# Kernel tuning notes

Hardware: AMD Instinct MI355X
Metric: run time of the kernel (lower is better)

Reference implementation:

```python
import jax, jax.numpy as jnp
import numpy as np

N_NODES = 50000
N_EDGES = 600000
D_IN = 128
D_HID = 128
D_OUT = 128
LN_EPS = 1e-5


def _layer_norm(h, g, b):
    mu = jnp.mean(h, axis=-1, keepdims=True)
    var = jnp.var(h, axis=-1, keepdims=True)
    return (h - mu) * jax.lax.rsqrt(var + LN_EPS) * g + b


def _gin_conv(x, src, dst, w1, b1, w2, b2):
    # sum-aggregate neighbor messages at destination nodes, eps = 0
    agg = jax.ops.segment_sum(x[src], dst, num_segments=x.shape[0])
    h = x + agg
    h = jax.nn.relu(h @ w1 + b1)
    return h @ w2 + b2


def setup_inputs() -> dict:
    key = jax.random.key(0)
    ks = jax.random.split(key, 20)
    x = jax.random.normal(ks[0], (N_NODES, D_IN), dtype=jnp.float32)
    edge_index = jax.random.randint(ks[1], (2, N_EDGES), 0, N_NODES, dtype=jnp.int64)
    dims = [(D_IN, D_HID), (D_HID, D_HID), (D_HID, D_HID), (D_HID, D_OUT)]
    inp = {"x": x, "edge_index": edge_index}
    for i, (din, dout) in enumerate(dims):
        s1 = 1.0 / np.sqrt(din)
        s2 = 1.0 / np.sqrt(D_HID)
        inp[f"w1_{i}"] = jax.random.uniform(ks[2 + 4 * i], (din, D_HID), jnp.float32, -s1, s1)
        inp[f"b1_{i}"] = jax.random.uniform(ks[3 + 4 * i], (D_HID,), jnp.float32, -s1, s1)
        inp[f"w2_{i}"] = jax.random.uniform(ks[4 + 4 * i], (D_HID, dout), jnp.float32, -s2, s2)
        inp[f"b2_{i}"] = jax.random.uniform(ks[5 + 4 * i], (dout,), jnp.float32, -s2, s2)
    for i in range(3):  # LayerNorm only on first 3 blocks
        inp[f"g_{i}"] = jnp.ones((D_HID,), jnp.float32)
        inp[f"beta_{i}"] = jnp.zeros((D_HID,), jnp.float32)
    return inp


def reference(x, edge_index,
              w1_0, b1_0, w2_0, b2_0,
              w1_1, b1_1, w2_1, b2_1,
              w1_2, b1_2, w2_2, b2_2,
              w1_3, b1_3, w2_3, b2_3,
              g_0, beta_0, g_1, beta_1, g_2, beta_2):
    src, dst = edge_index[0], edge_index[1]
    mlps = [(w1_0, b1_0, w2_0, b2_0), (w1_1, b1_1, w2_1, b2_1),
            (w1_2, b1_2, w2_2, b2_2), (w1_3, b1_3, w2_3, b2_3)]
    lns = [(g_0, beta_0), (g_1, beta_1), (g_2, beta_2)]
    h = x
    for i in range(3):
        h = _gin_conv(h, src, dst, *mlps[i])
        h = _layer_norm(h, *lns[i])
        h = jax.nn.relu(h)  # dropout rate 0.0 -> identity
    h = _gin_conv(h, src, dst, *mlps[3])  # final block: no norm/act
    return h
```

## Files before the change

### kernel.cpp

```cpp
#include <hip/hip_runtime.h>
#include <hip/hip_bf16.h>

#define NN 50000
#define NE 600000
#define DD 128
#define LDSW 136
#define SC 256
#define NCH ((NN + SC - 1) / SC)

typedef __bf16 bf16;
typedef __attribute__((ext_vector_type(8))) __bf16 bf16x8;
typedef __attribute__((ext_vector_type(4))) float f32x4;
typedef __attribute__((ext_vector_type(4))) unsigned int u32x4;
typedef __attribute__((ext_vector_type(4))) unsigned short u16x4;
typedef unsigned short u16;

__device__ __forceinline__ float bf_lo(unsigned int u) {
    return __builtin_bit_cast(float, u << 16);
}
__device__ __forceinline__ float bf_hi(unsigned int u) {
    return __builtin_bit_cast(float, u & 0xffff0000u);
}
__device__ __forceinline__ unsigned int bf_pack(float x, float y) {
    u16 a = __builtin_bit_cast(u16, (bf16)x);
    u16 b = __builtin_bit_cast(u16, (bf16)y);
    return (unsigned int)a | ((unsigned int)b << 16);
}

struct Ptr8 { const float* p[8]; };

__device__ __forceinline__ int edge_dst(const int* ei, int e, int f) {
    return f ? ei[2 * NE + 2 * e] : ei[NE + e];
}
__device__ __forceinline__ int edge_src(const int* ei, int e, int f) {
    return f ? ei[2 * e] : ei[e];
}

#define J0 50000
#define J1 (J0 + NN * DD / 4)
#define J2 (J1 + 8 * DD * DD)

__global__ __launch_bounds__(256) void k_init(const float* __restrict__ x,
                                              u16* __restrict__ xb,
                                              Ptr8 ws, u16* __restrict__ wt,
                                              int* __restrict__ deg,
                                              const int* __restrict__ ei,
                                              int* __restrict__ flag) {
    int tid = threadIdx.x;
    if (blockIdx.x == 0) {
        if (tid == 0) flag[0] = 1;
        __syncthreads();
        if (ei[2 * tid + 1] != 0) flag[0] = 0;
    }
    int id = blockIdx.x * 256 + tid;
    if (id < J0) {
        deg[id] = 0;
    } else if (id < J1) {
        int i = id - J0;
        f32x4 v = *(const f32x4*)(x + (size_t)i * 4);
        u16x4 o;
        o.x = __builtin_bit_cast(u16, (bf16)v.x);
        o.y = __builtin_bit_cast(u16, (bf16)v.y);
        o.z = __builtin_bit_cast(u16, (bf16)v.z);
        o.w = __builtin_bit_cast(u16, (bf16)v.w);
        *(u16x4*)(xb + (size_t)i * 4) = o;
    } else if (id < J2) {
        int i = id - J1;
        int m = i >> 14;
        int rem = i & 16383;
        int k = rem >> 7;
        int n = rem & 127;
        bf16 b = (bf16)ws.p[m][k * DD + n];
        wt[(size_t)m * DD * DD + n * DD + k] = __builtin_bit_cast(u16, b);
    }
}

__global__ void k_degree(const int* __restrict__ ei, const int* __restrict__ flag,
                         int* __restrict__ deg) {
    int i = blockIdx.x * blockDim.x + threadIdx.x;
    if (i < NE) {
        int f = flag[0];
        atomicAdd(&deg[edge_dst(ei, i, f)], 1);
    }
}

__global__ __launch_bounds__(256) void k_scan1(const int* __restrict__ deg,
                                               int* __restrict__ partial) {
    int b = blockIdx.x, tid = threadIdx.x;
    int i = b * SC + tid;
    int v = (i < NN) ? deg[i] : 0;
#pragma unroll
    for (int off = 1; off < 64; off <<= 1) v += __shfl_xor(v, off);
    __shared__ int sm[4];
    if ((tid & 63) == 0) sm[tid >> 6] = v;
    __syncthreads();
    if (tid == 0) partial[b] = sm[0] + sm[1] + sm[2] + sm[3];
}

__global__ __launch_bounds__(256) void k_scan2(const int* __restrict__ partial,
                                               int* __restrict__ chunk_off) {
    int tid = threadIdx.x;
    int lane = tid & 63, w = tid >> 6;
    int v = (tid < NCH) ? partial[tid] : 0;
    int orig = v;
#pragma unroll
    for (int off = 1; off < 64; off <<= 1) {
        int t = __shfl_up(v, off);
        if (lane >= off) v += t;
    }
    __shared__ int sm[4];
    if (lane == 63) sm[w] = v;
    __syncthreads();
    int add = 0;
    for (int k = 0; k < w; k++) add += sm[k];
    v += add;
    if (tid < NCH) chunk_off[tid] = v - orig;
}

__global__ __launch_bounds__(256) void k_scan3(const int* __restrict__ deg,
                                               const int* __restrict__ chunk_off,
                                               int* __restrict__ row_start,
                                               int* __restrict__ cursor) {
    int b = blockIdx.x, tid = threadIdx.x;
    int i = b * SC + tid;
    int lane = tid & 63, w = tid >> 6;
    int v = (i < NN) ? deg[i] : 0;
    int orig = v;
#pragma unroll
    for (int off = 1; off < 64; off <<= 1) {
        int t = __shfl_up(v, off);
        if (lane >= off) v += t;
    }
    __shared__ int sm[4];
    if (lane == 63) sm[w] = v;
    __syncthreads();
    int add = chunk_off[b];
    for (int k = 0; k < w; k++) add += sm[k];
    int ex = v - orig + add;
    if (i < NN) { row_start[i] = ex; cursor[i] = ex; }
    if (b == 0 && tid == 0) row_start[NN] = NE;
}

__global__ void k_fill(const int* __restrict__ ei, const int* __restrict__ flag,
                       int* __restrict__ cursor, int* __restrict__ adj) {
    int i = blockIdx.x * blockDim.x + threadIdx.x;
    if (i < NE) {
        int f = flag[0];
        int d = edge_dst(ei, i, f);
        int p = atomicAdd(&cursor[d], 1);
        adj[p] = edge_src(ei, i, f);
    }
}

__global__ __launch_bounds__(256) void k_agg(const u16* __restrict__ xb,
                                             const int* __restrict__ row_start,
                                             const int* __restrict__ adj,
                                             u16* __restrict__ out) {
    int gid = blockIdx.x * blockDim.x + threadIdx.x;
    int wave = gid >> 6, lane = gid & 63;
    int g = lane >> 4, l = lane & 15;
    int node = wave * 4 + g;
    if (node >= NN) return;
    const u32x4* base = (const u32x4*)xb;
    u32x4 sv = base[(size_t)node * 16 + l];
    float af[8];
#pragma unroll
    for (int j = 0; j < 4; j++) { af[2 * j] = bf_lo(sv[j]); af[2 * j + 1] = bf_hi(sv[j]); }
    int s = row_start[node], e = row_start[node + 1];
    int i = s;
    for (; i + 1 < e; i += 2) {
        u32x4 t0 = base[(size_t)adj[i] * 16 + l];
        u32x4 t1 = base[(size_t)adj[i + 1] * 16 + l];
#pragma unroll
        for (int j = 0; j < 4; j++) {
            af[2 * j]     += bf_lo(t0[j]) + bf_lo(t1[j]);
            af[2 * j + 1] += bf_hi(t0[j]) + bf_hi(t1[j]);
        }
    }
    if (i < e) {
        u32x4 t = base[(size_t)adj[i] * 16 + l];
#pragma unroll
        for (int j = 0; j < 4; j++) { af[2 * j] += bf_lo(t[j]); af[2 * j + 1] += bf_hi(t[j]); }
    }
    u32x4 o;
#pragma unroll
    for (int j = 0; j < 4; j++) o[j] = bf_pack(af[2 * j], af[2 * j + 1]);
    ((u32x4*)out)[(size_t)node * 16 + l] = o;
}

template <bool LN, bool B16OUT>
__global__ __launch_bounds__(256) void k_mlp(const u16* __restrict__ hin,
                                             const u16* __restrict__ w1t,
                                             const float* __restrict__ b1,
                                             const u16* __restrict__ w2t,
                                             const float* __restrict__ b2,
                                             const float* __restrict__ g,
                                             const float* __restrict__ bta,
                                             void* __restrict__ hout) {
    __shared__ u16 lds[128 * LDSW];
    const int tid = threadIdx.x;
    const int wv = tid >> 6, lane = tid & 63;
    const int l15 = lane & 15, l4 = lane >> 4;
    const int tile0 = blockIdx.x * 128;

#pragma unroll
    for (int it = 0; it < 8; ++it) {
        int slot = tid + it * 256;
        int row = slot >> 4, c16 = slot & 15;
        u32x4 v = {0u, 0u, 0u, 0u};
        int grow = tile0 + row;
        if (grow < NN) v = *(const u32x4*)(hin + (size_t)grow * DD + c16 * 8);
        *(u32x4*)&lds[row * LDSW + c16 * 8] = v;
    }
    __syncthreads();

    float b1c[8], b2c[8], gc[8], bc[8];
#pragma unroll
    for (int c = 0; c < 8; c++) {
        int col = c * 16 + l15;
        b1c[c] = b1[col];
        b2c[c] = b2[col];
        if (LN) { gc[c] = g[col]; bc[c] = bta[col]; }
    }

    f32x4 acc[2][8];
#pragma unroll
    for (int r = 0; r < 2; r++)
#pragma unroll
        for (int c = 0; c < 8; c++) acc[r][c] = (f32x4){0.f, 0.f, 0.f, 0.f};

    const int rowbase = wv * 32;

#pragma unroll
    for (int ks = 0; ks < 4; ++ks) {
        bf16x8 a0 = __builtin_bit_cast(bf16x8,
            *(const u32x4*)&lds[(rowbase + l15) * LDSW + ks * 32 + l4 * 8]);
        bf16x8 a1 = __builtin_bit_cast(bf16x8,
            *(const u32x4*)&lds[(rowbase + 16 + l15) * LDSW + ks * 32 + l4 * 8]);
#pragma unroll
        for (int c = 0; c < 8; c++) {
            bf16x8 b = __builtin_bit_cast(bf16x8,
                *(const u32x4*)(w1t + (size_t)(c * 16 + l15) * DD + ks * 32 + l4 * 8));
            acc[0][c] = __builtin_amdgcn_mfma_f32_16x16x32_bf16(a0, b, acc[0][c], 0, 0, 0);
            acc[1][c] = __builtin_amdgcn_mfma_f32_16x16x32_bf16(a1, b, acc[1][c], 0, 0, 0);
        }
    }

#pragma unroll
    for (int r = 0; r < 2; r++) {
#pragma unroll
        for (int c = 0; c < 8; c++) {
            int col = c * 16 + l15;
#pragma unroll
            for (int j = 0; j < 4; j++) {
                float v = acc[r][c][j] + b1c[c];
                v = v > 0.f ? v : 0.f;
                bf16 b = (bf16)v;
                int row = rowbase + r * 16 + l4 * 4 + j;
                lds[row * LDSW + col] = __builtin_bit_cast(u16, b);
            }
        }
    }
    __syncthreads();

#pragma unroll
    for (int r = 0; r < 2; r++)
#pragma unroll
        for (int c = 0; c < 8; c++) acc[r][c] = (f32x4){0.f, 0.f, 0.f, 0.f};

#pragma unroll
    for (int ks = 0; ks < 4; ++ks) {
        bf16x8 a0 = __builtin_bit_cast(bf16x8,
            *(const u32x4*)&lds[(rowbase + l15) * LDSW + ks * 32 + l4 * 8]);
        bf16x8 a1 = __builtin_bit_cast(bf16x8,
            *(const u32x4*)&lds[(rowbase + 16 + l15) * LDSW + ks * 32 + l4 * 8]);
#pragma unroll
        for (int c = 0; c < 8; c++) {
            bf16x8 b = __builtin_bit_cast(bf16x8,
                *(const u32x4*)(w2t + (size_t)(c * 16 + l15) * DD + ks * 32 + l4 * 8));
            acc[0][c] = __builtin_amdgcn_mfma_f32_16x16x32_bf16(a0, b, acc[0][c], 0, 0, 0);
            acc[1][c] = __builtin_amdgcn_mfma_f32_16x16x32_bf16(a1, b, acc[1][c], 0, 0, 0);
        }
    }

#pragma unroll
    for (int r = 0; r < 2; r++) {
        float vals[8][4];
#pragma unroll
        for (int c = 0; c < 8; c++)
#pragma unroll
            for (int j = 0; j < 4; j++) vals[c][j] = acc[r][c][j] + b2c[c];

        if (LN) {
            float s[4], q[4];
#pragma unroll
            for (int j = 0; j < 4; j++) {
                s[j] = 0.f; q[j] = 0.f;
#pragma unroll
                for (int c = 0; c < 8; c++) {
                    s[j] += vals[c][j];
                    q[j] += vals[c][j] * vals[c][j];
                }
            }
#pragma unroll
            for (int m = 1; m <= 8; m <<= 1) {
#pragma unroll
                for (int j = 0; j < 4; j++) {
                    s[j] += __shfl_xor(s[j], m);
                    q[j] += __shfl_xor(q[j], m);
                }
            }
#pragma unroll
            for (int j = 0; j < 4; j++) {
                float mu = s[j] * (1.f / 128.f);
                float var = q[j] * (1.f / 128.f) - mu * mu;
                float rs = rsqrtf(var + 1e-5f);
#pragma unroll
                for (int c = 0; c < 8; c++) {
                    float v = (vals[c][j] - mu) * rs * gc[c] + bc[c];
                    vals[c][j] = v > 0.f ? v : 0.f;
                }
            }
        }

#pragma unroll
        for (int c = 0; c < 8; c++) {
            int col = c * 16 + l15;
#pragma unroll
            for (int j = 0; j < 4; j++) {
                int row = tile0 + rowbase + r * 16 + l4 * 4 + j;
                if (row < NN) {
                    if (B16OUT) {
                        ((u16*)hout)[(size_t)row * DD + col] =
                            __builtin_bit_cast(u16, (bf16)vals[c][j]);
                    } else {
                        ((float*)hout)[(size_t)row * DD + col] = vals[c][j];
                    }
                }
            }
        }
    }
}

extern "C" void kernel_launch(void* const* d_in, const int* in_sizes, int n_in,
                              void* d_out, int out_size, void* d_ws, size_t ws_size,
                              hipStream_t stream) {
    const float* x = (const float*)d_in[0];
    const int* ei = (const int*)d_in[1];
    const float* w1[4]; const float* b1[4]; const float* w2[4]; const float* b2[4];
    for (int i = 0; i < 4; i++) {
        w1[i] = (const float*)d_in[2 + 4 * i];
        b1[i] = (const float*)d_in[3 + 4 * i];
        w2[i] = (const float*)d_in[4 + 4 * i];
        b2[i] = (const float*)d_in[5 + 4 * i];
    }
    const float* g[3]; const float* bt[3];
    for (int i = 0; i < 3; i++) {
        g[i] = (const float*)d_in[18 + 2 * i];
        bt[i] = (const float*)d_in[19 + 2 * i];
    }

    char* ws = (char*)d_ws;
    size_t off = 0;
    auto alloc = [&](size_t bytes) -> char* {
        char* p = ws + off;
        off = (off + bytes + 255) & ~(size_t)255;
        return p;
    };
    int* flag      = (int*)alloc(4);
    int* row_start = (int*)alloc((NN + 1) * 4);
    int* deg       = (int*)alloc(NN * 4);
    int* cursor    = (int*)alloc(NN * 4);
    int* adj       = (int*)alloc(NE * 4);
    int* partial   = (int*)alloc(NCH * 4);
    int* chunk_off = (int*)alloc(NCH * 4);
    u16* wt        = (u16*)alloc((size_t)8 * DD * DD * 2);
    u16* xb        = (u16*)alloc((size_t)NN * DD * 2);
    u16* hbf       = (u16*)alloc((size_t)NN * DD * 2);
    u16* hA        = (u16*)alloc((size_t)NN * DD * 2);
    u16* hB        = (u16*)alloc((size_t)NN * DD * 2);

    Ptr8 p8;
    for (int i = 0; i < 4; i++) {
        p8.p[2 * i] = w1[i];
        p8.p[2 * i + 1] = w2[i];
    }

    k_init<<<(J2 + 255) / 256, 256, 0, stream>>>(x, xb, p8, wt, deg, ei, flag);
    k_degree<<<(NE + 255) / 256, 256, 0, stream>>>(ei, flag, deg);
    k_scan1<<<NCH, 256, 0, stream>>>(deg, partial);
    k_scan2<<<1, 256, 0, stream>>>(partial, chunk_off);
    k_scan3<<<NCH, 256, 0, stream>>>(deg, chunk_off, row_start, cursor);
    k_fill<<<(NE + 255) / 256, 256, 0, stream>>>(ei, flag, cursor, adj);

    const u16* hin = xb;
    for (int i = 0; i < 4; i++) {
        k_agg<<<(NN / 4 * 64 + 255) / 256, 256, 0, stream>>>(hin, row_start, adj, hbf);
        const u16* w1ti = wt + (size_t)(2 * i) * DD * DD;
        const u16* w2ti = wt + (size_t)(2 * i + 1) * DD * DD;
        if (i < 3) {
            u16* outp = (i & 1) ? hB : hA;
            k_mlp<true, true><<<(NN + 127) / 128, 256, 0, stream>>>(
                hbf, w1ti, b1[i], w2ti, b2[i], g[i], bt[i], outp);
            hin = outp;
        } else {
            k_mlp<false, false><<<(NN + 127) / 128, 256, 0, stream>>>(
                hbf, w1ti, b1[i], w2ti, b2[i], nullptr, nullptr, d_out);
        }
    }
}
```

Measured before the change: 276.3 us.

## Fuse neighbor aggregation into MLP kernel, gathering directly into LDS

```diff
diff --git a/kernel.cpp b/kernel.cpp
--- a/kernel.cpp
+++ b/kernel.cpp
@@ -152,65 +152,61 @@
     }
 }
 
-__global__ __launch_bounds__(256) void k_agg(const u16* __restrict__ xb,
-                                             const int* __restrict__ row_start,
-                                             const int* __restrict__ adj,
-                                             u16* __restrict__ out) {
-    int gid = blockIdx.x * blockDim.x + threadIdx.x;
-    int wave = gid >> 6, lane = gid & 63;
-    int g = lane >> 4, l = lane & 15;
-    int node = wave * 4 + g;
-    if (node >= NN) return;
-    const u32x4* base = (const u32x4*)xb;
-    u32x4 sv = base[(size_t)node * 16 + l];
-    float af[8];
-#pragma unroll
-    for (int j = 0; j < 4; j++) { af[2 * j] = bf_lo(sv[j]); af[2 * j + 1] = bf_hi(sv[j]); }
-    int s = row_start[node], e = row_start[node + 1];
-    int i = s;
-    for (; i + 1 < e; i += 2) {
-        u32x4 t0 = base[(size_t)adj[i] * 16 + l];
-        u32x4 t1 = base[(size_t)adj[i + 1] * 16 + l];
-#pragma unroll
-        for (int j = 0; j < 4; j++) {
-            af[2 * j]     += bf_lo(t0[j]) + bf_lo(t1[j]);
-            af[2 * j + 1] += bf_hi(t0[j]) + bf_hi(t1[j]);
-        }
-    }
-    if (i < e) {
-        u32x4 t = base[(size_t)adj[i] * 16 + l];
-#pragma unroll
-        for (int j = 0; j < 4; j++) { af[2 * j] += bf_lo(t[j]); af[2 * j + 1] += bf_hi(t[j]); }
-    }
-    u32x4 o;
-#pragma unroll
-    for (int j = 0; j < 4; j++) o[j] = bf_pack(af[2 * j], af[2 * j + 1]);
-    ((u32x4*)out)[(size_t)node * 16 + l] = o;
-}
-
 template <bool LN, bool B16OUT>
-__global__ __launch_bounds__(256) void k_mlp(const u16* __restrict__ hin,
-                                             const u16* __restrict__ w1t,
-                                             const float* __restrict__ b1,
-                                             const u16* __restrict__ w2t,
-                                             const float* __restrict__ b2,
-                                             const float* __restrict__ g,
-                                             const float* __restrict__ bta,
-                                             void* __restrict__ hout) {
+__global__ __launch_bounds__(256) void k_fused(const u16* __restrict__ hin,
+                                               const int* __restrict__ row_start,
+                                               const int* __restrict__ adj,
+                                               const u16* __restrict__ w1t,
+                                               const float* __restrict__ b1,
+                                               const u16* __restrict__ w2t,
+                                               const float* __restrict__ b2,
+                                               const float* __restrict__ g,
+                                               const float* __restrict__ bta,
+                                               void* __restrict__ hout) {
     __shared__ u16 lds[128 * LDSW];
     const int tid = threadIdx.x;
     const int wv = tid >> 6, lane = tid & 63;
+    const int grp = lane >> 4, l = lane & 15;
     const int l15 = lane & 15, l4 = lane >> 4;
     const int tile0 = blockIdx.x * 128;
 
-#pragma unroll
-    for (int it = 0; it < 8; ++it) {
-        int slot = tid + it * 256;
-        int row = slot >> 4, c16 = slot & 15;
-        u32x4 v = {0u, 0u, 0u, 0u};
-        int grow = tile0 + row;
-        if (grow < NN) v = *(const u32x4*)(hin + (size_t)grow * DD + c16 * 8);
-        *(u32x4*)&lds[row * LDSW + c16 * 8] = v;
+    const u32x4* base = (const u32x4*)hin;
+#pragma unroll
+    for (int pass = 0; pass < 8; ++pass) {
+        int r = wv * 32 + pass * 4 + grp;
+        int node = tile0 + r;
+        float af[8], bf[8];
+#pragma unroll
+        for (int j = 0; j < 8; j++) { af[j] = 0.f; bf[j] = 0.f; }
+        if (node < NN) {
+            u32x4 sv = base[(size_t)node * 16 + l];
+#pragma unroll
+            for (int j = 0; j < 4; j++) { af[2 * j] = bf_lo(sv[j]); af[2 * j + 1] = bf_hi(sv[j]); }
+            int s = row_start[node], e = row_start[node + 1];
+            int i = s;
+            for (; i + 3 < e; i += 4) {
+                u32x4 t0 = base[(size_t)adj[i] * 16 + l];
+                u32x4 t1 = base[(size_t)adj[i + 1] * 16 + l];
+                u32x4 t2 = base[(size_t)adj[i + 2] * 16 + l];
+                u32x4 t3 = base[(size_t)adj[i + 3] * 16 + l];
+#pragma unroll
+                for (int j = 0; j < 4; j++) {
+                    af[2 * j]     += bf_lo(t0[j]) + bf_lo(t1[j]);
+                    af[2 * j + 1] += bf_hi(t0[j]) + bf_hi(t1[j]);
+                    bf[2 * j]     += bf_lo(t2[j]) + bf_lo(t3[j]);
+                    bf[2 * j + 1] += bf_hi(t2[j]) + bf_hi(t3[j]);
+                }
+            }
+            for (; i < e; i++) {
+                u32x4 t = base[(size_t)adj[i] * 16 + l];
+#pragma unroll
+                for (int j = 0; j < 4; j++) { af[2 * j] += bf_lo(t[j]); af[2 * j + 1] += bf_hi(t[j]); }
+            }
+        }
+        u32x4 o;
+#pragma unroll
+        for (int j = 0; j < 4; j++) o[j] = bf_pack(af[2 * j] + bf[2 * j], af[2 * j + 1] + bf[2 * j + 1]);
+        *(u32x4*)&lds[r * LDSW + l * 8] = o;
     }
     __syncthreads();
 
@@ -376,7 +372,6 @@
     int* chunk_off = (int*)alloc(NCH * 4);
     u16* wt        = (u16*)alloc((size_t)8 * DD * DD * 2);
     u16* xb        = (u16*)alloc((size_t)NN * DD * 2);
-    u16* hbf       = (u16*)alloc((size_t)NN * DD * 2);
     u16* hA        = (u16*)alloc((size_t)NN * DD * 2);
     u16* hB        = (u16*)alloc((size_t)NN * DD * 2);
 
@@ -393,19 +388,19 @@
     k_scan3<<<NCH, 256, 0, stream>>>(deg, chunk_off, row_start, cursor);
     k_fill<<<(NE + 255) / 256, 256, 0, stream>>>(ei, flag, cursor, adj);
 
+    const int grid = (NN + 127) / 128;
     const u16* hin = xb;
     for (int i = 0; i < 4; i++) {
-        k_agg<<<(NN / 4 * 64 + 255) / 256, 256, 0, stream>>>(hin, row_start, adj, hbf);
         const u16* w1ti = wt + (size_t)(2 * i) * DD * DD;
         const u16* w2ti = wt + (size_t)(2 * i + 1) * DD * DD;
         if (i < 3) {
             u16* outp = (i & 1) ? hB : hA;
-            k_mlp<true, true><<<(NN + 127) / 128, 256, 0, stream>>>(
-                hbf, w1ti, b1[i], w2ti, b2[i], g[i], bt[i], outp);
+            k_fused<true, true><<<grid, 256, 0, stream>>>(
+                hin, row_start, adj, w1ti, b1[i], w2ti, b2[i], g[i], bt[i], outp);
             hin = outp;
         } else {
-            k_mlp<false, false><<<(NN + 127) / 128, 256, 0, stream>>>(
-                hbf, w1ti, b1[i], w2ti, b2[i], nullptr, nullptr, d_out);
-        }
-    }
-}
+            k_fused<false, false><<<grid, 256, 0, stream>>>(
+                hin, row_start, adj, w1ti, b1[i], w2ti, b2[i], nullptr, nullptr, d_out);
+        }
+    }
+}
```

After: 322.7 us. 16.8% more time.

## Sort nodes by degree for aggregation and unroll gather loop by four

Applied to the files above, without the earlier changes.

```diff
diff --git a/kernel.cpp b/kernel.cpp
--- a/kernel.cpp
+++ b/kernel.cpp
@@ -7,6 +7,7 @@
 #define LDSW 136
 #define SC 256
 #define NCH ((NN + SC - 1) / SC)
+#define NBIN 64
 
 typedef __bf16 bf16;
 typedef __attribute__((ext_vector_type(8))) __bf16 bf16x8;
@@ -44,6 +45,7 @@
                                               u16* __restrict__ xb,
                                               Ptr8 ws, u16* __restrict__ wt,
                                               int* __restrict__ deg,
+                                              int* __restrict__ hist,
                                               const int* __restrict__ ei,
                                               int* __restrict__ flag) {
     int tid = threadIdx.x;
@@ -53,6 +55,7 @@
         if (ei[2 * tid + 1] != 0) flag[0] = 0;
     }
     int id = blockIdx.x * 256 + tid;
+    if (id < NBIN) hist[id] = 0;
     if (id < J0) {
         deg[id] = 0;
     } else if (id < J1) {
@@ -85,20 +88,32 @@
 }
 
 __global__ __launch_bounds__(256) void k_scan1(const int* __restrict__ deg,
-                                               int* __restrict__ partial) {
+                                               int* __restrict__ partial,
+                                               int* __restrict__ hist) {
     int b = blockIdx.x, tid = threadIdx.x;
     int i = b * SC + tid;
     int v = (i < NN) ? deg[i] : 0;
-#pragma unroll
-    for (int off = 1; off < 64; off <<= 1) v += __shfl_xor(v, off);
+    __shared__ int lh[NBIN];
+    if (tid < NBIN) lh[tid] = 0;
+    __syncthreads();
+    if (i < NN) {
+        int d = v > (NBIN - 1) ? (NBIN - 1) : v;
+        atomicAdd(&lh[d], 1);
+    }
+    int s = v;
+#pragma unroll
+    for (int off = 1; off < 64; off <<= 1) s += __shfl_xor(s, off);
     __shared__ int sm[4];
-    if ((tid & 63) == 0) sm[tid >> 6] = v;
+    if ((tid & 63) == 0) sm[tid >> 6] = s;
     __syncthreads();
     if (tid == 0) partial[b] = sm[0] + sm[1] + sm[2] + sm[3];
+    if (tid < NBIN && lh[tid] > 0) atomicAdd(&hist[tid], lh[tid]);
 }
 
 __global__ __launch_bounds__(256) void k_scan2(const int* __restrict__ partial,
-                                               int* __restrict__ chunk_off) {
+                                               int* __restrict__ chunk_off,
+                                               const int* __restrict__ hist,
+                                               int* __restrict__ dcur) {
     int tid = threadIdx.x;
     int lane = tid & 63, w = tid >> 6;
     int v = (tid < NCH) ? partial[tid] : 0;
@@ -115,12 +130,24 @@
     for (int k = 0; k < w; k++) add += sm[k];
     v += add;
     if (tid < NCH) chunk_off[tid] = v - orig;
+    if (tid < NBIN) {
+        int h = hist[tid];
+        int hv = h;
+#pragma unroll
+        for (int off = 1; off < 64; off <<= 1) {
+            int t = __shfl_up(hv, off);
+            if (lane >= off) hv += t;
+        }
+        dcur[tid] = hv - h;
+    }
 }
 
 __global__ __launch_bounds__(256) void k_scan3(const int* __restrict__ deg,
                                                const int* __restrict__ chunk_off,
                                                int* __restrict__ row_start,
-                                               int* __restrict__ cursor) {
+                                               int* __restrict__ cursor,
+                                               int* __restrict__ dcur,
+                                               int* __restrict__ perm) {
     int b = blockIdx.x, tid = threadIdx.x;
     int i = b * SC + tid;
     int lane = tid & 63, w = tid >> 6;
@@ -139,6 +166,20 @@
     int ex = v - orig + add;
     if (i < NN) { row_start[i] = ex; cursor[i] = ex; }
     if (b == 0 && tid == 0) row_start[NN] = NE;
+
+    __shared__ int lh[NBIN];
+    __shared__ int gb[NBIN];
+    if (tid < NBIN) lh[tid] = 0;
+    __syncthreads();
+    int d = 0, lpos = 0;
+    if (i < NN) {
+        d = orig > (NBIN - 1) ? (NBIN - 1) : orig;
+        lpos = atomicAdd(&lh[d], 1);
+    }
+    __syncthreads();
+    if (tid < NBIN && lh[tid] > 0) gb[tid] = atomicAdd(&dcur[tid], lh[tid]);
+    __syncthreads();
+    if (i < NN) perm[gb[d] + lpos] = i;
 }
 
 __global__ void k_fill(const int* __restrict__ ei, const int* __restrict__ flag,
@@ -155,36 +196,44 @@
 __global__ __launch_bounds__(256) void k_agg(const u16* __restrict__ xb,
                                              const int* __restrict__ row_start,
                                              const int* __restrict__ adj,
+                                             const int* __restrict__ perm,
                                              u16* __restrict__ out) {
     int gid = blockIdx.x * blockDim.x + threadIdx.x;
     int wave = gid >> 6, lane = gid & 63;
-    int g = lane >> 4, l = lane & 15;
-    int node = wave * 4 + g;
-    if (node >= NN) return;
+    int grp = lane >> 4, l = lane & 15;
+    int slot = wave * 4 + grp;
+    int node = perm[slot];
     const u32x4* base = (const u32x4*)xb;
     u32x4 sv = base[(size_t)node * 16 + l];
-    float af[8];
-#pragma unroll
-    for (int j = 0; j < 4; j++) { af[2 * j] = bf_lo(sv[j]); af[2 * j + 1] = bf_hi(sv[j]); }
+    float af[8], bf[8];
+#pragma unroll
+    for (int j = 0; j < 4; j++) {
+        af[2 * j] = bf_lo(sv[j]); af[2 * j + 1] = bf_hi(sv[j]);
+        bf[2 * j] = 0.f; bf[2 * j + 1] = 0.f;
+    }
     int s = row_start[node], e = row_start[node + 1];
     int i = s;
-    for (; i + 1 < e; i += 2) {
+    for (; i + 3 < e; i += 4) {
         u32x4 t0 = base[(size_t)adj[i] * 16 + l];
         u32x4 t1 = base[(size_t)adj[i + 1] * 16 + l];
+        u32x4 t2 = base[(size_t)adj[i + 2] * 16 + l];
+        u32x4 t3 = base[(size_t)adj[i + 3] * 16 + l];
 #pragma unroll
         for (int j = 0; j < 4; j++) {
             af[2 * j]     += bf_lo(t0[j]) + bf_lo(t1[j]);
             af[2 * j + 1] += bf_hi(t0[j]) + bf_hi(t1[j]);
-        }
-    }
-    if (i < e) {
+            bf[2 * j]     += bf_lo(t2[j]) + bf_lo(t3[j]);
+            bf[2 * j + 1] += bf_hi(t2[j]) + bf_hi(t3[j]);
+        }
+    }
+    for (; i < e; i++) {
         u32x4 t = base[(size_t)adj[i] * 16 + l];
 #pragma unroll
         for (int j = 0; j < 4; j++) { af[2 * j] += bf_lo(t[j]); af[2 * j + 1] += bf_hi(t[j]); }
     }
     u32x4 o;
 #pragma unroll
-    for (int j = 0; j < 4; j++) o[j] = bf_pack(af[2 * j], af[2 * j + 1]);
+    for (int j = 0; j < 4; j++) o[j] = bf_pack(af[2 * j] + bf[2 * j], af[2 * j + 1] + bf[2 * j + 1]);
     ((u32x4*)out)[(size_t)node * 16 + l] = o;
 }
 
@@ -374,6 +423,9 @@
     int* adj       = (int*)alloc(NE * 4);
     int* partial   = (int*)alloc(NCH * 4);
     int* chunk_off = (int*)alloc(NCH * 4);
+    int* hist      = (int*)alloc(NBIN * 4);
+    int* dcur      = (int*)alloc(NBIN * 4);
+    int* perm      = (int*)alloc(NN * 4);
     u16* wt        = (u16*)alloc((size_t)8 * DD * DD * 2);
     u16* xb        = (u16*)alloc((size_t)NN * DD * 2);
     u16* hbf       = (u16*)alloc((size_t)NN * DD * 2);
@@ -386,16 +438,16 @@
         p8.p[2 * i + 1] = w2[i];
     }
 
-    k_init<<<(J2 + 255) / 256, 256, 0, stream>>>(x, xb, p8, wt, deg, ei, flag);
+    k_init<<<(J2 + 255) / 256, 256, 0, stream>>>(x, xb, p8, wt, deg, hist, ei, flag);
     k_degree<<<(NE + 255) / 256, 256, 0, stream>>>(ei, flag, deg);
-    k_scan1<<<NCH, 256, 0, stream>>>(deg, partial);
-    k_scan2<<<1, 256, 0, stream>>>(partial, chunk_off);
-    k_scan3<<<NCH, 256, 0, stream>>>(deg, chunk_off, row_start, cursor);
+    k_scan1<<<NCH, 256, 0, stream>>>(deg, partial, hist);
+    k_scan2<<<1, 256, 0, stream>>>(partial, chunk_off, hist, dcur);
+    k_scan3<<<NCH, 256, 0, stream>>>(deg, chunk_off, row_start, cursor, dcur, perm);
     k_fill<<<(NE + 255) / 256, 256, 0, stream>>>(ei, flag, cursor, adj);
 
     const u16* hin = xb;
     for (int i = 0; i < 4; i++) {
-        k_agg<<<(NN / 4 * 64 + 255) / 256, 256, 0, stream>>>(hin, row_start, adj, hbf);
+        k_agg<<<(NN / 4 * 64) / 256, 256, 0, stream>>>(hin, row_start, adj, perm, hbf);
         const u16* w1ti = wt + (size_t)(2 * i) * DD * DD;
         const u16* w2ti = wt + (size_t)(2 * i + 1) * DD * DD;
         if (i < 3) {
```

Result: no change. 276.6 us (+0.1%).

## Build CSR via two-level bucket sort instead of global atomic degree counting

Applied to the files above, without the earlier changes.

```diff
diff --git a/kernel.cpp b/kernel.cpp
--- a/kernel.cpp
+++ b/kernel.cpp
@@ -5,8 +5,10 @@
 #define NE 600000
 #define DD 128
 #define LDSW 136
-#define SC 256
-#define NCH ((NN + SC - 1) / SC)
+#define NB 196
+#define BSH 8
+#define EPB 2048
+#define NBLK_AC ((NE + EPB - 1) / EPB)
 
 typedef __bf16 bf16;
 typedef __attribute__((ext_vector_type(8))) __bf16 bf16x8;
@@ -36,14 +38,13 @@
     return f ? ei[2 * e] : ei[e];
 }
 
-#define J0 50000
-#define J1 (J0 + NN * DD / 4)
+#define J1 (NN * DD / 4)
 #define J2 (J1 + 8 * DD * DD)
 
 __global__ __launch_bounds__(256) void k_init(const float* __restrict__ x,
                                               u16* __restrict__ xb,
                                               Ptr8 ws, u16* __restrict__ wt,
-                                              int* __restrict__ deg,
+                                              int* __restrict__ bcnt,
                                               const int* __restrict__ ei,
                                               int* __restrict__ flag) {
     int tid = threadIdx.x;
@@ -53,17 +54,15 @@
         if (ei[2 * tid + 1] != 0) flag[0] = 0;
     }
     int id = blockIdx.x * 256 + tid;
-    if (id < J0) {
-        deg[id] = 0;
-    } else if (id < J1) {
-        int i = id - J0;
-        f32x4 v = *(const f32x4*)(x + (size_t)i * 4);
+    if (id < NB) bcnt[id] = 0;
+    if (id < J1) {
+        f32x4 v = *(const f32x4*)(x + (size_t)id * 4);
         u16x4 o;
         o.x = __builtin_bit_cast(u16, (bf16)v.x);
         o.y = __builtin_bit_cast(u16, (bf16)v.y);
         o.z = __builtin_bit_cast(u16, (bf16)v.z);
         o.w = __builtin_bit_cast(u16, (bf16)v.w);
-        *(u16x4*)(xb + (size_t)i * 4) = o;
+        *(u16x4*)(xb + (size_t)id * 4) = o;
     } else if (id < J2) {
         int i = id - J1;
         int m = i >> 14;
@@ -75,33 +74,32 @@
     }
 }
 
-__global__ void k_degree(const int* __restrict__ ei, const int* __restrict__ flag,
-                         int* __restrict__ deg) {
-    int i = blockIdx.x * blockDim.x + threadIdx.x;
-    if (i < NE) {
-        int f = flag[0];
-        atomicAdd(&deg[edge_dst(ei, i, f)], 1);
-    }
-}
-
-__global__ __launch_bounds__(256) void k_scan1(const int* __restrict__ deg,
-                                               int* __restrict__ partial) {
-    int b = blockIdx.x, tid = threadIdx.x;
-    int i = b * SC + tid;
-    int v = (i < NN) ? deg[i] : 0;
-#pragma unroll
-    for (int off = 1; off < 64; off <<= 1) v += __shfl_xor(v, off);
-    __shared__ int sm[4];
-    if ((tid & 63) == 0) sm[tid >> 6] = v;
-    __syncthreads();
-    if (tid == 0) partial[b] = sm[0] + sm[1] + sm[2] + sm[3];
-}
-
-__global__ __launch_bounds__(256) void k_scan2(const int* __restrict__ partial,
-                                               int* __restrict__ chunk_off) {
+__global__ __launch_bounds__(256) void k_bcount(const int* __restrict__ ei,
+                                                const int* __restrict__ flag,
+                                                int* __restrict__ bcnt) {
+    __shared__ int lh[NB];
+    int tid = threadIdx.x;
+    if (tid < NB) lh[tid] = 0;
+    __syncthreads();
+    int f = flag[0];
+#pragma unroll
+    for (int k = 0; k < 8; k++) {
+        int e = blockIdx.x * EPB + k * 256 + tid;
+        if (e < NE) {
+            int d = edge_dst(ei, e, f);
+            atomicAdd(&lh[d >> BSH], 1);
+        }
+    }
+    __syncthreads();
+    if (tid < NB && lh[tid] > 0) atomicAdd(&bcnt[tid], lh[tid]);
+}
+
+__global__ __launch_bounds__(256) void k_bscan(const int* __restrict__ bcnt,
+                                               int* __restrict__ boff,
+                                               int* __restrict__ bcur) {
     int tid = threadIdx.x;
     int lane = tid & 63, w = tid >> 6;
-    int v = (tid < NCH) ? partial[tid] : 0;
+    int v = (tid < NB) ? bcnt[tid] : 0;
     int orig = v;
 #pragma unroll
     for (int off = 1; off < 64; off <<= 1) {
@@ -113,42 +111,82 @@
     __syncthreads();
     int add = 0;
     for (int k = 0; k < w; k++) add += sm[k];
-    v += add;
-    if (tid < NCH) chunk_off[tid] = v - orig;
-}
-
-__global__ __launch_bounds__(256) void k_scan3(const int* __restrict__ deg,
-                                               const int* __restrict__ chunk_off,
+    int ex = v - orig + add;
+    if (tid < NB) { boff[tid] = ex; bcur[tid] = ex; }
+    if (tid == 0) boff[NB] = NE;
+}
+
+__global__ __launch_bounds__(256) void k_bscatter(const int* __restrict__ ei,
+                                                  const int* __restrict__ flag,
+                                                  int* __restrict__ bcur,
+                                                  uint2* __restrict__ tmp) {
+    __shared__ int lh[NB];
+    __shared__ int gb[NB];
+    int tid = threadIdx.x;
+    if (tid < NB) lh[tid] = 0;
+    __syncthreads();
+    int f = flag[0];
+    int src[8], dst[8], lp[8];
+    bool val[8];
+#pragma unroll
+    for (int k = 0; k < 8; k++) {
+        int e = blockIdx.x * EPB + k * 256 + tid;
+        val[k] = (e < NE);
+        if (val[k]) {
+            src[k] = edge_src(ei, e, f);
+            dst[k] = edge_dst(ei, e, f);
+            lp[k] = atomicAdd(&lh[dst[k] >> BSH], 1);
+        }
+    }
+    __syncthreads();
+    if (tid < NB && lh[tid] > 0) gb[tid] = atomicAdd(&bcur[tid], lh[tid]);
+    __syncthreads();
+#pragma unroll
+    for (int k = 0; k < 8; k++) {
+        if (val[k]) {
+            uint2 pr; pr.x = (unsigned)src[k]; pr.y = (unsigned)dst[k];
+            tmp[gb[dst[k] >> BSH] + lp[k]] = pr;
+        }
+    }
+}
+
+__global__ __launch_bounds__(256) void k_build(const uint2* __restrict__ tmp,
+                                               const int* __restrict__ boff,
                                                int* __restrict__ row_start,
-                                               int* __restrict__ cursor) {
+                                               int* __restrict__ adj) {
+    __shared__ int cnt[256];
+    __shared__ int ccur[256];
+    __shared__ int sm[4];
     int b = blockIdx.x, tid = threadIdx.x;
-    int i = b * SC + tid;
+    int base = b << BSH;
+    int s = boff[b], e = boff[b + 1];
+    cnt[tid] = 0;
+    __syncthreads();
+    for (int i = s + tid; i < e; i += 256) {
+        atomicAdd(&cnt[tmp[i].y - base], 1);
+    }
+    __syncthreads();
+    int v = cnt[tid];
+    int orig = v;
     int lane = tid & 63, w = tid >> 6;
-    int v = (i < NN) ? deg[i] : 0;
-    int orig = v;
 #pragma unroll
     for (int off = 1; off < 64; off <<= 1) {
         int t = __shfl_up(v, off);
         if (lane >= off) v += t;
     }
-    __shared__ int sm[4];
     if (lane == 63) sm[w] = v;
     __syncthreads();
-    int add = chunk_off[b];
+    int add = 0;
     for (int k = 0; k < w; k++) add += sm[k];
-    int ex = v - orig + add;
-    if (i < NN) { row_start[i] = ex; cursor[i] = ex; }
+    int ex = s + (v - orig) + add;
+    ccur[tid] = ex;
+    if (base + tid < NN) row_start[base + tid] = ex;
     if (b == 0 && tid == 0) row_start[NN] = NE;
-}
-
-__global__ void k_fill(const int* __restrict__ ei, const int* __restrict__ flag,
-                       int* __restrict__ cursor, int* __restrict__ adj) {
-    int i = blockIdx.x * blockDim.x + threadIdx.x;
-    if (i < NE) {
-        int f = flag[0];
-        int d = edge_dst(ei, i, f);
-        int p = atomicAdd(&cursor[d], 1);
-        adj[p] = edge_src(ei, i, f);
+    __syncthreads();
+    for (int i = s + tid; i < e; i += 256) {
+        uint2 pr = tmp[i];
+        int p = atomicAdd(&ccur[pr.y - base], 1);
+        adj[p] = (int)pr.x;
     }
 }
 
@@ -158,33 +196,40 @@
                                              u16* __restrict__ out) {
     int gid = blockIdx.x * blockDim.x + threadIdx.x;
     int wave = gid >> 6, lane = gid & 63;
-    int g = lane >> 4, l = lane & 15;
-    int node = wave * 4 + g;
+    int grp = lane >> 4, l = lane & 15;
+    int node = wave * 4 + grp;
     if (node >= NN) return;
     const u32x4* base = (const u32x4*)xb;
     u32x4 sv = base[(size_t)node * 16 + l];
-    float af[8];
-#pragma unroll
-    for (int j = 0; j < 4; j++) { af[2 * j] = bf_lo(sv[j]); af[2 * j + 1] = bf_hi(sv[j]); }
+    float af[8], bf[8];
+#pragma unroll
+    for (int j = 0; j < 4; j++) {
+        af[2 * j] = bf_lo(sv[j]); af[2 * j + 1] = bf_hi(sv[j]);
+        bf[2 * j] = 0.f; bf[2 * j + 1] = 0.f;
+    }
     int s = row_start[node], e = row_start[node + 1];
     int i = s;
-    for (; i + 1 < e; i += 2) {
+    for (; i + 3 < e; i += 4) {
         u32x4 t0 = base[(size_t)adj[i] * 16 + l];
         u32x4 t1 = base[(size_t)adj[i + 1] * 16 + l];
+        u32x4 t2 = base[(size_t)adj[i + 2] * 16 + l];
+        u32x4 t3 = base[(size_t)adj[i + 3] * 16 + l];
 #pragma unroll
         for (int j = 0; j < 4; j++) {
             af[2 * j]     += bf_lo(t0[j]) + bf_lo(t1[j]);
             af[2 * j + 1] += bf_hi(t0[j]) + bf_hi(t1[j]);
-        }
-    }
-    if (i < e) {
+            bf[2 * j]     += bf_lo(t2[j]) + bf_lo(t3[j]);
+            bf[2 * j + 1] += bf_hi(t2[j]) + bf_hi(t3[j]);
+        }
+    }
+    for (; i < e; i++) {
         u32x4 t = base[(size_t)adj[i] * 16 + l];
 #pragma unroll
         for (int j = 0; j < 4; j++) { af[2 * j] += bf_lo(t[j]); af[2 * j + 1] += bf_hi(t[j]); }
     }
     u32x4 o;
 #pragma unroll
-    for (int j = 0; j < 4; j++) o[j] = bf_pack(af[2 * j], af[2 * j + 1]);
+    for (int j = 0; j < 4; j++) o[j] = bf_pack(af[2 * j] + bf[2 * j], af[2 * j + 1] + bf[2 * j + 1]);
     ((u32x4*)out)[(size_t)node * 16 + l] = o;
 }
 
@@ -369,11 +414,11 @@
     };
     int* flag      = (int*)alloc(4);
     int* row_start = (int*)alloc((NN + 1) * 4);
-    int* deg       = (int*)alloc(NN * 4);
-    int* cursor    = (int*)alloc(NN * 4);
+    int* bcnt      = (int*)alloc(NB * 4);
+    int* boff      = (int*)alloc((NB + 1) * 4);
+    int* bcur      = (int*)alloc(NB * 4);
     int* adj       = (int*)alloc(NE * 4);
-    int* partial   = (int*)alloc(NCH * 4);
-    int* chunk_off = (int*)alloc(NCH * 4);
+    uint2* tmp     = (uint2*)alloc((size_t)NE * 8);
     u16* wt        = (u16*)alloc((size_t)8 * DD * DD * 2);
     u16* xb        = (u16*)alloc((size_t)NN * DD * 2);
     u16* hbf       = (u16*)alloc((size_t)NN * DD * 2);
@@ -386,16 +431,15 @@
         p8.p[2 * i + 1] = w2[i];
     }
 
-    k_init<<<(J2 + 255) / 256, 256, 0, stream>>>(x, xb, p8, wt, deg, ei, flag);
-    k_degree<<<(NE + 255) / 256, 256, 0, stream>>>(ei, flag, deg);
-    k_scan1<<<NCH, 256, 0, stream>>>(deg, partial);
-    k_scan2<<<1, 256, 0, stream>>>(partial, chunk_off);
-    k_scan3<<<NCH, 256, 0, stream>>>(deg, chunk_off, row_start, cursor);
-    k_fill<<<(NE + 255) / 256, 256, 0, stream>>>(ei, flag, cursor, adj);
+    k_init<<<(J2 + 255) / 256, 256, 0, stream>>>(x, xb, p8, wt, bcnt, ei, flag);
+    k_bcount<<<NBLK_AC, 256, 0, stream>>>(ei, flag, bcnt);
+    k_bscan<<<1, 256, 0, stream>>>(bcnt, boff, bcur);
+    k_bscatter<<<NBLK_AC, 256, 0, stream>>>(ei, flag, bcur, tmp);
+    k_build<<<NB, 256, 0, stream>>>(tmp, boff, row_start, adj);
 
     const u16* hin = xb;
     for (int i = 0; i < 4; i++) {
-        k_agg<<<(NN / 4 * 64 + 255) / 256, 256, 0, stream>>>(hin, row_start, adj, hbf);
+        k_agg<<<(NN / 4 * 64) / 256, 256, 0, stream>>>(hin, row_start, adj, hbf);
         const u16* w1ti = wt + (size_t)(2 * i) * DD * DD;
         const u16* w2ti = wt + (size_t)(2 * i + 1) * DD * DD;
         if (i < 3) {
```

Result: faster. 235.5 us (-14.8%).
